# Kernel tuning notes

Hardware: AMD Instinct MI355X
Metric: run time of the kernel (lower is better)

The kernel has to match this reference:

```python
import jax, jax.numpy as jnp
import numpy as np

B, N, D = 256, 512, 128   # meta_batch, num_sample, feat_dim; in_c = 2*D = 256, base_c = 128
EPS_L1 = 1e-12
EPS_BN = 1e-5
NEG_SLOPE = 0.01


def setup_inputs() -> dict:
    key = jax.random.key(0)
    ks = jax.random.split(key, 6)
    return {
        "distribution_edge": jax.random.uniform(ks[0], (B, N, N), dtype=jnp.float32),
        "instance_edge": jax.random.uniform(ks[1], (B, N, N), dtype=jnp.float32),
        "point_node": jax.random.normal(ks[2], (B, N, D), dtype=jnp.float32),
        "W1": jax.random.normal(ks[3], (2 * D, 2 * D), dtype=jnp.float32) * 0.05,  # Conv2d 1x1: (out_c=base_c*2, in_c)
        "g1": jnp.ones((2 * D,), jnp.float32),
        "b1": jnp.zeros((2 * D,), jnp.float32),
        "W2": jax.random.normal(ks[4], (D, 2 * D), dtype=jnp.float32) * 0.05,     # Conv2d 1x1: (out_c=base_c, base_c*2)
        "g2": jnp.ones((D,), jnp.float32),
        "b2": jnp.zeros((D,), jnp.float32),
    }


def _l1_normalize(x):
    # F.normalize(x, p=1, dim=-1): x / max(sum(|x|, -1), 1e-12)
    return x / jnp.clip(jnp.sum(jnp.abs(x), axis=-1, keepdims=True), EPS_L1, None)


def _bn_lrelu(x, g, b):
    # x: (B, C, N); BatchNorm2d training-mode stats over (batch, spatial), biased var
    mean = jnp.mean(x, axis=(0, 2), keepdims=True)
    var = jnp.var(x, axis=(0, 2), keepdims=True)
    y = (x - mean) * jax.lax.rsqrt(var + EPS_BN) * g[None, :, None] + b[None, :, None]
    return jnp.where(y >= 0, y, NEG_SLOPE * y)


def reference(distribution_edge, instance_edge, point_node, W1, g1, b1, W2, g2, b2):
    n = point_node.shape[1]
    diag_mask = 1.0 - jnp.eye(n, dtype=point_node.dtype)  # broadcasts over meta_batch
    edge_feat = _l1_normalize(distribution_edge * diag_mask)
    aggr_feat = jnp.einsum('bij,bjd->bid', edge_feat, point_node)
    edge_instance = _l1_normalize(instance_edge * diag_mask)
    aggr_instance = jnp.einsum('bij,bjd->bid', edge_instance, point_node)
    x = jnp.concatenate([aggr_feat, aggr_instance], axis=-1)  # (B, N, 2D)
    x = jnp.swapaxes(x, 1, 2)                                  # (B, 2D, N)
    h = _bn_lrelu(jnp.einsum('oc,bcn->bon', W1, x), g1, b1)    # 1x1 conv, no bias
    h = _bn_lrelu(jnp.einsum('oc,bcn->bon', W2, h), g2, b2)
    return jnp.swapaxes(h, 1, 2)                               # (B, N, base_c)
```

## Files before the change

### kernel.cpp

```cpp
#include <hip/hip_runtime.h>
#include <hip/hip_bf16.h>
#include <string.h>

#define BB 256
#define NNS 512
#define DDF 128
#define CC1 256
#define CC2 128
#define NPOS (BB * NNS)

typedef __attribute__((ext_vector_type(4))) float f32x4;
typedef __attribute__((ext_vector_type(8))) short bf16x8;

__device__ __forceinline__ short f2bf(float f) {
    __hip_bfloat16 h = __float2bfloat16(f);
    short s;
    __builtin_memcpy(&s, &h, 2);
    return s;
}
__device__ __forceinline__ float bf2f(short s) {
    unsigned int u = ((unsigned int)(unsigned short)s) << 16;
    float f;
    __builtin_memcpy(&f, &u, 4);
    return f;
}
__device__ __forceinline__ unsigned int pk2bf(float a, float b) {
    float2 t; t.x = a; t.y = b;
    __hip_bfloat162 h = __float22bfloat162_rn(t);
    unsigned int u;
    __builtin_memcpy(&u, &h, 4);
    return u;
}

#define MFMA16(a, b, c) __builtin_amdgcn_mfma_f32_16x16x32_bf16(a, b, c, 0, 0, 0)

__global__ void prep_kernel(const float* __restrict__ W1, const float* __restrict__ W2,
                            short* __restrict__ W1b, short* __restrict__ W2b,
                            float* __restrict__ stats) {
    int idx = blockIdx.x * 256 + threadIdx.x;
    if (idx < CC1 * CC1) W1b[idx] = f2bf(W1[idx]);
    if (idx < CC2 * CC1) W2b[idx] = f2bf(W2[idx]);
    if (idx < 1536) stats[idx] = 0.0f;
}

__global__ __launch_bounds__(256) void transposeP_kernel(const float* __restrict__ P,
                                                         short* __restrict__ PT) {
    __shared__ float tp[64 * 132];
    int b = blockIdx.x >> 3;
    int j0 = (blockIdx.x & 7) * 64;
    int t = threadIdx.x;
    const float* Pb = P + ((size_t)b * NNS + j0) * DDF;
    int jr = t >> 5, dc = (t & 31) * 4;
#pragma unroll
    for (int p = 0; p < 8; ++p) {
        int j = p * 8 + jr;
        float4 v = *reinterpret_cast<const float4*>(&Pb[(size_t)j * DDF + dc]);
        *reinterpret_cast<float4*>(&tp[j * 132 + dc]) = v;
    }
    __syncthreads();
    int jo = t & 7;
#pragma unroll
    for (int p = 0; p < 4; ++p) {
        int d = p * 32 + (t >> 3);
        bf16x8 v;
#pragma unroll
        for (int s = 0; s < 8; ++s) v[s] = f2bf(tp[(jo * 8 + s) * 132 + d]);
        *reinterpret_cast<bf16x8*>(&PT[((size_t)(b * DDF + d)) * NNS + j0 + jo * 8]) = v;
    }
}

__global__ __launch_bounds__(256) void gemm1_kernel(const float* __restrict__ dE,
                                                    const float* __restrict__ iE,
                                                    const short* __restrict__ PT,
                                                    short* __restrict__ X) {
    int bid = blockIdx.x;
    int mtb = bid & 3;
    int e = (bid >> 2) & 1;
    int b = bid >> 3;
    const float* E = (e == 0 ? dE : iE) + (size_t)b * (NNS * NNS);
    const short* PTb = PT + (size_t)b * (DDF * NNS);

    int tid = threadIdx.x;
    int lane = tid & 63, w = tid >> 6;
    int quad = lane >> 4, lr = lane & 15;
    int rbase = mtb * 128 + w * 32;

    const float* Ap[2];
#pragma unroll
    for (int mt = 0; mt < 2; ++mt)
        Ap[mt] = E + (size_t)(rbase + mt * 16 + lr) * NNS + quad * 8;
    const short* Bp[8];
#pragma unroll
    for (int nt = 0; nt < 8; ++nt)
        Bp[nt] = PTb + (size_t)(nt * 16 + lr) * NNS + quad * 8;

    f32x4 zero = {0.f, 0.f, 0.f, 0.f};
    f32x4 acc[2][8];
#pragma unroll
    for (int a = 0; a < 2; ++a)
#pragma unroll
        for (int c = 0; c < 8; ++c) acc[a][c] = zero;
    float rs[2] = {0.f, 0.f};

    float4 pa0[2], pa1[2];
#pragma unroll
    for (int mt = 0; mt < 2; ++mt) {
        pa0[mt] = *reinterpret_cast<const float4*>(Ap[mt]);
        pa1[mt] = *reinterpret_cast<const float4*>(Ap[mt] + 4);
    }
    int kkd = rbase >> 5;

#pragma unroll 2
    for (int kk = 0; kk < 16; ++kk) {
        bf16x8 bv[8];
#pragma unroll
        for (int nt = 0; nt < 8; ++nt)
            bv[nt] = *reinterpret_cast<const bf16x8*>(Bp[nt] + kk * 32);
#pragma unroll
        for (int mt = 0; mt < 2; ++mt) {
            float4 v0 = pa0[mt], v1 = pa1[mt];
            if (kk < 15) {
                pa0[mt] = *reinterpret_cast<const float4*>(Ap[mt] + (kk + 1) * 32);
                pa1[mt] = *reinterpret_cast<const float4*>(Ap[mt] + (kk + 1) * 32 + 4);
            }
            float a8[8] = {v0.x, v0.y, v0.z, v0.w, v1.x, v1.y, v1.z, v1.w};
            if (kk == kkd) {
                int t = (mt << 4) + lr;
#pragma unroll
                for (int tt = 0; tt < 8; ++tt)
                    if (quad * 8 + tt == t) a8[tt] = 0.0f;
            }
            float s = rs[mt];
#pragma unroll
            for (int tt = 0; tt < 8; ++tt) s += fabsf(a8[tt]);
            rs[mt] = s;
            union { bf16x8 v; unsigned int u[4]; } af;
#pragma unroll
            for (int tt = 0; tt < 4; ++tt) af.u[tt] = pk2bf(a8[2 * tt], a8[2 * tt + 1]);
#pragma unroll
            for (int nt = 0; nt < 8; ++nt)
                acc[mt][nt] = MFMA16(af.v, bv[nt], acc[mt][nt]);
        }
    }

#pragma unroll
    for (int mt = 0; mt < 2; ++mt) {
        float s = rs[mt];
        s += __shfl_xor(s, 16, 64);
        s += __shfl_xor(s, 32, 64);
        float inv = 1.0f / fmaxf(s, 1e-12f);
        float ir[4];
#pragma unroll
        for (int r = 0; r < 4; ++r) ir[r] = __shfl(inv, quad * 4 + r, 64);
#pragma unroll
        for (int nt = 0; nt < 8; ++nt) {
            int col = e * 128 + nt * 16 + lr;
#pragma unroll
            for (int r = 0; r < 4; ++r) {
                int row = rbase + mt * 16 + quad * 4 + r;
                X[((size_t)b * NNS + row) * CC1 + col] = f2bf(acc[mt][nt][r] * ir[r]);
            }
        }
    }
}

__global__ __launch_bounds__(512) void gemm2_kernel(const short* __restrict__ X,
                                                    const short* __restrict__ W1b,
                                                    short* __restrict__ Y1,
                                                    float* __restrict__ sum1,
                                                    float* __restrict__ sumsq1) {
    int pbase = blockIdx.x * 128;
    int tid = threadIdx.x;
    int lane = tid & 63, w = tid >> 6;
    int quad = lane >> 4, lr = lane & 15;
    int mh = w >> 2, nh = w & 3;

    const short* Ap[4];
#pragma unroll
    for (int mt = 0; mt < 4; ++mt)
        Ap[mt] = X + (size_t)(pbase + mh * 64 + mt * 16 + lr) * CC1 + quad * 8;
    const short* Bp[4];
#pragma unroll
    for (int nt = 0; nt < 4; ++nt)
        Bp[nt] = W1b + (size_t)(nh * 64 + nt * 16 + lr) * CC1 + quad * 8;

    f32x4 zero = {0.f, 0.f, 0.f, 0.f};
    f32x4 acc[4][4];
#pragma unroll
    for (int a = 0; a < 4; ++a)
#pragma unroll
        for (int c = 0; c < 4; ++c) acc[a][c] = zero;

    bf16x8 pa[4];
#pragma unroll
    for (int mt = 0; mt < 4; ++mt) pa[mt] = *reinterpret_cast<const bf16x8*>(Ap[mt]);

#pragma unroll 2
    for (int kk = 0; kk < 8; ++kk) {
        bf16x8 bv[4];
#pragma unroll
        for (int nt = 0; nt < 4; ++nt)
            bv[nt] = *reinterpret_cast<const bf16x8*>(Bp[nt] + kk * 32);
#pragma unroll
        for (int mt = 0; mt < 4; ++mt) {
            bf16x8 av = pa[mt];
            if (kk < 7) pa[mt] = *reinterpret_cast<const bf16x8*>(Ap[mt] + (kk + 1) * 32);
#pragma unroll
            for (int nt = 0; nt < 4; ++nt) acc[mt][nt] = MFMA16(av, bv[nt], acc[mt][nt]);
        }
    }
#pragma unroll
    for (int nt = 0; nt < 4; ++nt) {
        int o = nh * 64 + nt * 16 + lr;
        float s = 0.f, q = 0.f;
#pragma unroll
        for (int mt = 0; mt < 4; ++mt)
#pragma unroll
            for (int r = 0; r < 4; ++r) {
                float v = acc[mt][nt][r];
                s += v;
                q += v * v;
            }
        s += __shfl_xor(s, 16, 64); s += __shfl_xor(s, 32, 64);
        q += __shfl_xor(q, 16, 64); q += __shfl_xor(q, 32, 64);
        if (lane < 16) {
            atomicAdd(&sum1[o], s);
            atomicAdd(&sumsq1[o], q);
        }
#pragma unroll
        for (int mt = 0; mt < 4; ++mt)
#pragma unroll
            for (int r = 0; r < 4; ++r) {
                int pos = pbase + mh * 64 + mt * 16 + quad * 4 + r;
                Y1[(size_t)pos * CC1 + o] = f2bf(acc[mt][nt][r]);
            }
    }
}

__global__ void finalize_kernel(const float* __restrict__ sum, const float* __restrict__ sumsq,
                                const float* __restrict__ g, const float* __restrict__ b,
                                float* __restrict__ scale, float* __restrict__ shift, int C) {
    int i = threadIdx.x;
    if (i < C) {
        const float invM = 1.0f / (float)NPOS;
        float m = sum[i] * invM;
        float v = sumsq[i] * invM - m * m;
        float s = g[i] * rsqrtf(v + 1e-5f);
        scale[i] = s;
        shift[i] = b[i] - m * s;
    }
}

__global__ __launch_bounds__(256) void gemm3_kernel(const short* __restrict__ Y1,
                                                    const short* __restrict__ W2b,
                                                    const float* __restrict__ scale1,
                                                    const float* __restrict__ shift1,
                                                    float* __restrict__ Y2,
                                                    float* __restrict__ sum2,
                                                    float* __restrict__ sumsq2) {
    __shared__ __align__(16) float ssc[CC1];
    __shared__ __align__(16) float ssh[CC1];
    ssc[threadIdx.x] = scale1[threadIdx.x];
    ssh[threadIdx.x] = shift1[threadIdx.x];
    __syncthreads();

    int pbase = blockIdx.x * 128;
    int tid = threadIdx.x;
    int lane = tid & 63, w = tid >> 6;
    int quad = lane >> 4, lr = lane & 15;
    int mh = w >> 1, nh = w & 1;

    const short* Ap[4];
#pragma unroll
    for (int mt = 0; mt < 4; ++mt)
        Ap[mt] = Y1 + (size_t)(pbase + mh * 64 + mt * 16 + lr) * CC1 + quad * 8;
    const short* Bp[4];
#pragma unroll
    for (int nt = 0; nt < 4; ++nt)
        Bp[nt] = W2b + (size_t)(nh * 64 + nt * 16 + lr) * CC1 + quad * 8;

    f32x4 zero = {0.f, 0.f, 0.f, 0.f};
    f32x4 acc[4][4];
#pragma unroll
    for (int a = 0; a < 4; ++a)
#pragma unroll
        for (int c = 0; c < 4; ++c) acc[a][c] = zero;

    bf16x8 pa[4];
#pragma unroll
    for (int mt = 0; mt < 4; ++mt) pa[mt] = *reinterpret_cast<const bf16x8*>(Ap[mt]);

#pragma unroll 2
    for (int kk = 0; kk < 8; ++kk) {
        bf16x8 bv[4];
#pragma unroll
        for (int nt = 0; nt < 4; ++nt)
            bv[nt] = *reinterpret_cast<const bf16x8*>(Bp[nt] + kk * 32);
        int k0 = kk * 32 + quad * 8;
        float4 sc0 = *reinterpret_cast<const float4*>(&ssc[k0]);
        float4 sc1 = *reinterpret_cast<const float4*>(&ssc[k0 + 4]);
        float4 sh0 = *reinterpret_cast<const float4*>(&ssh[k0]);
        float4 sh1 = *reinterpret_cast<const float4*>(&ssh[k0 + 4]);
        float scv[8] = {sc0.x, sc0.y, sc0.z, sc0.w, sc1.x, sc1.y, sc1.z, sc1.w};
        float shv[8] = {sh0.x, sh0.y, sh0.z, sh0.w, sh1.x, sh1.y, sh1.z, sh1.w};
#pragma unroll
        for (int mt = 0; mt < 4; ++mt) {
            bf16x8 raw = pa[mt];
            if (kk < 7) pa[mt] = *reinterpret_cast<const bf16x8*>(Ap[mt] + (kk + 1) * 32);
            union { bf16x8 v; unsigned int u[4]; } af;
#pragma unroll
            for (int tt = 0; tt < 4; ++tt) {
                float va = bf2f(raw[2 * tt]) * scv[2 * tt] + shv[2 * tt];
                va = fmaxf(va, 0.01f * va);
                float vb = bf2f(raw[2 * tt + 1]) * scv[2 * tt + 1] + shv[2 * tt + 1];
                vb = fmaxf(vb, 0.01f * vb);
                af.u[tt] = pk2bf(va, vb);
            }
#pragma unroll
            for (int nt = 0; nt < 4; ++nt) acc[mt][nt] = MFMA16(af.v, bv[nt], acc[mt][nt]);
        }
    }
#pragma unroll
    for (int nt = 0; nt < 4; ++nt) {
        int o = nh * 64 + nt * 16 + lr;
        float s = 0.f, q = 0.f;
#pragma unroll
        for (int mt = 0; mt < 4; ++mt)
#pragma unroll
            for (int r = 0; r < 4; ++r) {
                float v = acc[mt][nt][r];
                s += v;
                q += v * v;
            }
        s += __shfl_xor(s, 16, 64); s += __shfl_xor(s, 32, 64);
        q += __shfl_xor(q, 16, 64); q += __shfl_xor(q, 32, 64);
        if (lane < 16) {
            atomicAdd(&sum2[o], s);
            atomicAdd(&sumsq2[o], q);
        }
#pragma unroll
        for (int mt = 0; mt < 4; ++mt)
#pragma unroll
            for (int r = 0; r < 4; ++r) {
                int pos = pbase + mh * 64 + mt * 16 + quad * 4 + r;
                Y2[(size_t)pos * CC2 + o] = acc[mt][nt][r];
            }
    }
}

__global__ void apply2_kernel(const float* __restrict__ Y2, const float* __restrict__ scale2,
                              const float* __restrict__ shift2, float* __restrict__ out) {
    size_t gid = (size_t)blockIdx.x * 256 + threadIdx.x;
    size_t base = gid * 4;
    float4 y = *reinterpret_cast<const float4*>(&Y2[base]);
    int o = (int)(base & 127);
    float4 sc = *reinterpret_cast<const float4*>(&scale2[o]);
    float4 sh = *reinterpret_cast<const float4*>(&shift2[o]);
    float4 t;
    t.x = y.x * sc.x + sh.x; t.x = fmaxf(t.x, 0.01f * t.x);
    t.y = y.y * sc.y + sh.y; t.y = fmaxf(t.y, 0.01f * t.y);
    t.z = y.z * sc.z + sh.z; t.z = fmaxf(t.z, 0.01f * t.z);
    t.w = y.w * sc.w + sh.w; t.w = fmaxf(t.w, 0.01f * t.w);
    *reinterpret_cast<float4*>(&out[base]) = t;
}

extern "C" void kernel_launch(void* const* d_in, const int* in_sizes, int n_in,
                              void* d_out, int out_size, void* d_ws, size_t ws_size,
                              hipStream_t stream) {
    const float* dE = (const float*)d_in[0];
    const float* iE = (const float*)d_in[1];
    const float* P  = (const float*)d_in[2];
    const float* W1 = (const float*)d_in[3];
    const float* g1 = (const float*)d_in[4];
    const float* b1 = (const float*)d_in[5];
    const float* W2 = (const float*)d_in[6];
    const float* g2 = (const float*)d_in[7];
    const float* b2 = (const float*)d_in[8];
    float* out = (float*)d_out;
    char* ws = (char*)d_ws;

    short* PT  = (short*)(ws + 0);
    short* X   = (short*)(ws + 33554432);
    short* Y1  = (short*)(ws + 100663296);
    float* Y2  = (float*)(ws + 33554432);
    short* W1b = (short*)(ws + 167772160);
    short* W2b = (short*)(ws + 167903232);
    float* st  = (float*)(ws + 167968768);
    float* sum1 = st,        * sumsq1 = st + 256, * scale1 = st + 512,  * shift1 = st + 768;
    float* sum2 = st + 1024, * sumsq2 = st + 1152, * scale2 = st + 1280, * shift2 = st + 1408;

    prep_kernel<<<256, 256, 0, stream>>>(W1, W2, W1b, W2b, st);
    transposeP_kernel<<<2048, 256, 0, stream>>>(P, PT);
    gemm1_kernel<<<2048, 256, 0, stream>>>(dE, iE, PT, X);
    gemm2_kernel<<<1024, 512, 0, stream>>>(X, W1b, Y1, sum1, sumsq1);
    finalize_kernel<<<1, 256, 0, stream>>>(sum1, sumsq1, g1, b1, scale1, shift1, CC1);
    gemm3_kernel<<<1024, 256, 0, stream>>>(Y1, W2b, scale1, shift1, Y2, sum2, sumsq2);
    finalize_kernel<<<1, 128, 0, stream>>>(sum2, sumsq2, g2, b2, scale2, shift2, CC2);
    apply2_kernel<<<16384, 256, 0, stream>>>(Y2, scale2, shift2, out);
}
```

Measured before the change: 866.3 us.

## Shrink GEMM tiles and double-buffer operand loads in all three GEMM kernels

In the edge GEMM the four waves now split the tile into a 2x2 grid over rows and output columns, so each block covers 64 rows and 4096 blocks launch. The two pointwise GEMMs halve their row tile to 64 positions and launch twice as many blocks. All three kernels now prefetch A two k-steps ahead and B one step ahead into register double buffers, with the loops fully unrolled. The goal is to hide global-load latency and raise occupancy. The cost is that each edge row is now loaded by two waves, and the full unroll may increase register pressure.

```diff
diff --git a/kernel.cpp b/kernel.cpp
--- a/kernel.cpp
+++ b/kernel.cpp
@@ -74,55 +74,62 @@
                                                     const short* __restrict__ PT,
                                                     short* __restrict__ X) {
     int bid = blockIdx.x;
-    int mtb = bid & 3;
-    int e = (bid >> 2) & 1;
-    int b = bid >> 3;
+    int rt = bid & 7;
+    int e = (bid >> 3) & 1;
+    int b = bid >> 4;
     const float* E = (e == 0 ? dE : iE) + (size_t)b * (NNS * NNS);
     const short* PTb = PT + (size_t)b * (DDF * NNS);
 
     int tid = threadIdx.x;
     int lane = tid & 63, w = tid >> 6;
     int quad = lane >> 4, lr = lane & 15;
-    int rbase = mtb * 128 + w * 32;
+    int mh = w >> 1, nh = w & 1;
+    int rbase = rt * 64 + mh * 32;
 
     const float* Ap[2];
 #pragma unroll
     for (int mt = 0; mt < 2; ++mt)
         Ap[mt] = E + (size_t)(rbase + mt * 16 + lr) * NNS + quad * 8;
-    const short* Bp[8];
-#pragma unroll
-    for (int nt = 0; nt < 8; ++nt)
-        Bp[nt] = PTb + (size_t)(nt * 16 + lr) * NNS + quad * 8;
+    const short* Bp[4];
+#pragma unroll
+    for (int nt = 0; nt < 4; ++nt)
+        Bp[nt] = PTb + (size_t)(nh * 64 + nt * 16 + lr) * NNS + quad * 8;
 
     f32x4 zero = {0.f, 0.f, 0.f, 0.f};
-    f32x4 acc[2][8];
+    f32x4 acc[2][4];
 #pragma unroll
     for (int a = 0; a < 2; ++a)
 #pragma unroll
-        for (int c = 0; c < 8; ++c) acc[a][c] = zero;
+        for (int c = 0; c < 4; ++c) acc[a][c] = zero;
     float rs[2] = {0.f, 0.f};
 
-    float4 pa0[2], pa1[2];
+    float4 ab0[2][2], ab1[2][2];
+    bf16x8 bb[2][4];
 #pragma unroll
     for (int mt = 0; mt < 2; ++mt) {
-        pa0[mt] = *reinterpret_cast<const float4*>(Ap[mt]);
-        pa1[mt] = *reinterpret_cast<const float4*>(Ap[mt] + 4);
-    }
+        ab0[0][mt] = *reinterpret_cast<const float4*>(Ap[mt]);
+        ab1[0][mt] = *reinterpret_cast<const float4*>(Ap[mt] + 4);
+        ab0[1][mt] = *reinterpret_cast<const float4*>(Ap[mt] + 32);
+        ab1[1][mt] = *reinterpret_cast<const float4*>(Ap[mt] + 36);
+    }
+#pragma unroll
+    for (int nt = 0; nt < 4; ++nt)
+        bb[0][nt] = *reinterpret_cast<const bf16x8*>(Bp[nt]);
+
     int kkd = rbase >> 5;
 
-#pragma unroll 2
+#pragma unroll
     for (int kk = 0; kk < 16; ++kk) {
-        bf16x8 bv[8];
-#pragma unroll
-        for (int nt = 0; nt < 8; ++nt)
-            bv[nt] = *reinterpret_cast<const bf16x8*>(Bp[nt] + kk * 32);
+        int cb = kk & 1;
+        if (kk < 15) {
+#pragma unroll
+            for (int nt = 0; nt < 4; ++nt)
+                bb[cb ^ 1][nt] = *reinterpret_cast<const bf16x8*>(Bp[nt] + (kk + 1) * 32);
+        }
+        union { bf16x8 v; unsigned int u[4]; } af[2];
 #pragma unroll
         for (int mt = 0; mt < 2; ++mt) {
-            float4 v0 = pa0[mt], v1 = pa1[mt];
-            if (kk < 15) {
-                pa0[mt] = *reinterpret_cast<const float4*>(Ap[mt] + (kk + 1) * 32);
-                pa1[mt] = *reinterpret_cast<const float4*>(Ap[mt] + (kk + 1) * 32 + 4);
-            }
+            float4 v0 = ab0[cb][mt], v1 = ab1[cb][mt];
             float a8[8] = {v0.x, v0.y, v0.z, v0.w, v1.x, v1.y, v1.z, v1.w};
             if (kk == kkd) {
                 int t = (mt << 4) + lr;
@@ -134,13 +141,21 @@
 #pragma unroll
             for (int tt = 0; tt < 8; ++tt) s += fabsf(a8[tt]);
             rs[mt] = s;
-            union { bf16x8 v; unsigned int u[4]; } af;
-#pragma unroll
-            for (int tt = 0; tt < 4; ++tt) af.u[tt] = pk2bf(a8[2 * tt], a8[2 * tt + 1]);
-#pragma unroll
-            for (int nt = 0; nt < 8; ++nt)
-                acc[mt][nt] = MFMA16(af.v, bv[nt], acc[mt][nt]);
-        }
+#pragma unroll
+            for (int tt = 0; tt < 4; ++tt) af[mt].u[tt] = pk2bf(a8[2 * tt], a8[2 * tt + 1]);
+        }
+        if (kk < 14) {
+#pragma unroll
+            for (int mt = 0; mt < 2; ++mt) {
+                ab0[cb][mt] = *reinterpret_cast<const float4*>(Ap[mt] + (kk + 2) * 32);
+                ab1[cb][mt] = *reinterpret_cast<const float4*>(Ap[mt] + (kk + 2) * 32 + 4);
+            }
+        }
+#pragma unroll
+        for (int mt = 0; mt < 2; ++mt)
+#pragma unroll
+            for (int nt = 0; nt < 4; ++nt)
+                acc[mt][nt] = MFMA16(af[mt].v, bb[cb][nt], acc[mt][nt]);
     }
 
 #pragma unroll
@@ -153,8 +168,8 @@
 #pragma unroll
         for (int r = 0; r < 4; ++r) ir[r] = __shfl(inv, quad * 4 + r, 64);
 #pragma unroll
-        for (int nt = 0; nt < 8; ++nt) {
-            int col = e * 128 + nt * 16 + lr;
+        for (int nt = 0; nt < 4; ++nt) {
+            int col = e * 128 + nh * 64 + nt * 16 + lr;
 #pragma unroll
             for (int r = 0; r < 4; ++r) {
                 int row = rbase + mt * 16 + quad * 4 + r;
@@ -169,52 +184,66 @@
                                                     short* __restrict__ Y1,
                                                     float* __restrict__ sum1,
                                                     float* __restrict__ sumsq1) {
-    int pbase = blockIdx.x * 128;
+    int pbase = blockIdx.x * 64;
     int tid = threadIdx.x;
     int lane = tid & 63, w = tid >> 6;
     int quad = lane >> 4, lr = lane & 15;
     int mh = w >> 2, nh = w & 3;
 
-    const short* Ap[4];
-#pragma unroll
-    for (int mt = 0; mt < 4; ++mt)
-        Ap[mt] = X + (size_t)(pbase + mh * 64 + mt * 16 + lr) * CC1 + quad * 8;
+    const short* Ap[2];
+#pragma unroll
+    for (int mt = 0; mt < 2; ++mt)
+        Ap[mt] = X + (size_t)(pbase + mh * 32 + mt * 16 + lr) * CC1 + quad * 8;
     const short* Bp[4];
 #pragma unroll
     for (int nt = 0; nt < 4; ++nt)
         Bp[nt] = W1b + (size_t)(nh * 64 + nt * 16 + lr) * CC1 + quad * 8;
 
     f32x4 zero = {0.f, 0.f, 0.f, 0.f};
-    f32x4 acc[4][4];
-#pragma unroll
-    for (int a = 0; a < 4; ++a)
+    f32x4 acc[2][4];
+#pragma unroll
+    for (int a = 0; a < 2; ++a)
 #pragma unroll
         for (int c = 0; c < 4; ++c) acc[a][c] = zero;
 
-    bf16x8 pa[4];
-#pragma unroll
-    for (int mt = 0; mt < 4; ++mt) pa[mt] = *reinterpret_cast<const bf16x8*>(Ap[mt]);
-
-#pragma unroll 2
+    bf16x8 ab[2][2], bb[2][4];
+#pragma unroll
+    for (int mt = 0; mt < 2; ++mt) {
+        ab[0][mt] = *reinterpret_cast<const bf16x8*>(Ap[mt]);
+        ab[1][mt] = *reinterpret_cast<const bf16x8*>(Ap[mt] + 32);
+    }
+#pragma unroll
+    for (int nt = 0; nt < 4; ++nt)
+        bb[0][nt] = *reinterpret_cast<const bf16x8*>(Bp[nt]);
+
+#pragma unroll
     for (int kk = 0; kk < 8; ++kk) {
-        bf16x8 bv[4];
-#pragma unroll
-        for (int nt = 0; nt < 4; ++nt)
-            bv[nt] = *reinterpret_cast<const bf16x8*>(Bp[nt] + kk * 32);
-#pragma unroll
-        for (int mt = 0; mt < 4; ++mt) {
-            bf16x8 av = pa[mt];
-            if (kk < 7) pa[mt] = *reinterpret_cast<const bf16x8*>(Ap[mt] + (kk + 1) * 32);
-#pragma unroll
-            for (int nt = 0; nt < 4; ++nt) acc[mt][nt] = MFMA16(av, bv[nt], acc[mt][nt]);
-        }
+        int cb = kk & 1;
+        if (kk < 7) {
+#pragma unroll
+            for (int nt = 0; nt < 4; ++nt)
+                bb[cb ^ 1][nt] = *reinterpret_cast<const bf16x8*>(Bp[nt] + (kk + 1) * 32);
+        }
+        bf16x8 av[2];
+#pragma unroll
+        for (int mt = 0; mt < 2; ++mt) av[mt] = ab[cb][mt];
+        if (kk < 6) {
+#pragma unroll
+            for (int mt = 0; mt < 2; ++mt)
+                ab[cb][mt] = *reinterpret_cast<const bf16x8*>(Ap[mt] + (kk + 2) * 32);
+        }
+#pragma unroll
+        for (int mt = 0; mt < 2; ++mt)
+#pragma unroll
+            for (int nt = 0; nt < 4; ++nt)
+                acc[mt][nt] = MFMA16(av[mt], bb[cb][nt], acc[mt][nt]);
     }
 #pragma unroll
     for (int nt = 0; nt < 4; ++nt) {
         int o = nh * 64 + nt * 16 + lr;
         float s = 0.f, q = 0.f;
 #pragma unroll
-        for (int mt = 0; mt < 4; ++mt)
+        for (int mt = 0; mt < 2; ++mt)
 #pragma unroll
             for (int r = 0; r < 4; ++r) {
                 float v = acc[mt][nt][r];
@@ -228,10 +257,10 @@
             atomicAdd(&sumsq1[o], q);
         }
 #pragma unroll
-        for (int mt = 0; mt < 4; ++mt)
+        for (int mt = 0; mt < 2; ++mt)
 #pragma unroll
             for (int r = 0; r < 4; ++r) {
-                int pos = pbase + mh * 64 + mt * 16 + quad * 4 + r;
+                int pos = pbase + mh * 32 + mt * 16 + quad * 4 + r;
                 Y1[(size_t)pos * CC1 + o] = f2bf(acc[mt][nt][r]);
             }
     }
@@ -264,38 +293,46 @@
     ssh[threadIdx.x] = shift1[threadIdx.x];
     __syncthreads();
 
-    int pbase = blockIdx.x * 128;
+    int pbase = blockIdx.x * 64;
     int tid = threadIdx.x;
     int lane = tid & 63, w = tid >> 6;
     int quad = lane >> 4, lr = lane & 15;
     int mh = w >> 1, nh = w & 1;
 
-    const short* Ap[4];
-#pragma unroll
-    for (int mt = 0; mt < 4; ++mt)
-        Ap[mt] = Y1 + (size_t)(pbase + mh * 64 + mt * 16 + lr) * CC1 + quad * 8;
+    const short* Ap[2];
+#pragma unroll
+    for (int mt = 0; mt < 2; ++mt)
+        Ap[mt] = Y1 + (size_t)(pbase + mh * 32 + mt * 16 + lr) * CC1 + quad * 8;
     const short* Bp[4];
 #pragma unroll
     for (int nt = 0; nt < 4; ++nt)
         Bp[nt] = W2b + (size_t)(nh * 64 + nt * 16 + lr) * CC1 + quad * 8;
 
     f32x4 zero = {0.f, 0.f, 0.f, 0.f};
-    f32x4 acc[4][4];
-#pragma unroll
-    for (int a = 0; a < 4; ++a)
+    f32x4 acc[2][4];
+#pragma unroll
+    for (int a = 0; a < 2; ++a)
 #pragma unroll
         for (int c = 0; c < 4; ++c) acc[a][c] = zero;
 
-    bf16x8 pa[4];
-#pragma unroll
-    for (int mt = 0; mt < 4; ++mt) pa[mt] = *reinterpret_cast<const bf16x8*>(Ap[mt]);
-
-#pragma unroll 2
+    bf16x8 ab[2][2], bb[2][4];
+#pragma unroll
+    for (int mt = 0; mt < 2; ++mt) {
+        ab[0][mt] = *reinterpret_cast<const bf16x8*>(Ap[mt]);
+        ab[1][mt] = *reinterpret_cast<const bf16x8*>(Ap[mt] + 32);
+    }
+#pragma unroll
+    for (int nt = 0; nt < 4; ++nt)
+        bb[0][nt] = *reinterpret_cast<const bf16x8*>(Bp[nt]);
+
+#pragma unroll
     for (int kk = 0; kk < 8; ++kk) {
-        bf16x8 bv[4];
-#pragma unroll
-        for (int nt = 0; nt < 4; ++nt)
-            bv[nt] = *reinterpret_cast<const bf16x8*>(Bp[nt] + kk * 32);
+        int cb = kk & 1;
+        if (kk < 7) {
+#pragma unroll
+            for (int nt = 0; nt < 4; ++nt)
+                bb[cb ^ 1][nt] = *reinterpret_cast<const bf16x8*>(Bp[nt] + (kk + 1) * 32);
+        }
         int k0 = kk * 32 + quad * 8;
         float4 sc0 = *reinterpret_cast<const float4*>(&ssc[k0]);
         float4 sc1 = *reinterpret_cast<const float4*>(&ssc[k0 + 4]);
@@ -303,29 +340,36 @@
         float4 sh1 = *reinterpret_cast<const float4*>(&ssh[k0 + 4]);
         float scv[8] = {sc0.x, sc0.y, sc0.z, sc0.w, sc1.x, sc1.y, sc1.z, sc1.w};
         float shv[8] = {sh0.x, sh0.y, sh0.z, sh0.w, sh1.x, sh1.y, sh1.z, sh1.w};
-#pragma unroll
-        for (int mt = 0; mt < 4; ++mt) {
-            bf16x8 raw = pa[mt];
-            if (kk < 7) pa[mt] = *reinterpret_cast<const bf16x8*>(Ap[mt] + (kk + 1) * 32);
-            union { bf16x8 v; unsigned int u[4]; } af;
+        union { bf16x8 v; unsigned int u[4]; } af[2];
+#pragma unroll
+        for (int mt = 0; mt < 2; ++mt) {
+            bf16x8 raw = ab[cb][mt];
 #pragma unroll
             for (int tt = 0; tt < 4; ++tt) {
                 float va = bf2f(raw[2 * tt]) * scv[2 * tt] + shv[2 * tt];
                 va = fmaxf(va, 0.01f * va);
                 float vb = bf2f(raw[2 * tt + 1]) * scv[2 * tt + 1] + shv[2 * tt + 1];
                 vb = fmaxf(vb, 0.01f * vb);
-                af.u[tt] = pk2bf(va, vb);
-            }
-#pragma unroll
-            for (int nt = 0; nt < 4; ++nt) acc[mt][nt] = MFMA16(af.v, bv[nt], acc[mt][nt]);
-        }
+                af[mt].u[tt] = pk2bf(va, vb);
+            }
+        }
+        if (kk < 6) {
+#pragma unroll
+            for (int mt = 0; mt < 2; ++mt)
+                ab[cb][mt] = *reinterpret_cast<const bf16x8*>(Ap[mt] + (kk + 2) * 32);
+        }
+#pragma unroll
+        for (int mt = 0; mt < 2; ++mt)
+#pragma unroll
+            for (int nt = 0; nt < 4; ++nt)
+                acc[mt][nt] = MFMA16(af[mt].v, bb[cb][nt], acc[mt][nt]);
     }
 #pragma unroll
     for (int nt = 0; nt < 4; ++nt) {
         int o = nh * 64 + nt * 16 + lr;
         float s = 0.f, q = 0.f;
 #pragma unroll
-        for (int mt = 0; mt < 4; ++mt)
+        for (int mt = 0; mt < 2; ++mt)
 #pragma unroll
             for (int r = 0; r < 4; ++r) {
                 float v = acc[mt][nt][r];
@@ -339,10 +383,10 @@
             atomicAdd(&sumsq2[o], q);
         }
 #pragma unroll
-        for (int mt = 0; mt < 4; ++mt)
+        for (int mt = 0; mt < 2; ++mt)
 #pragma unroll
             for (int r = 0; r < 4; ++r) {
-                int pos = pbase + mh * 64 + mt * 16 + quad * 4 + r;
+                int pos = pbase + mh * 32 + mt * 16 + quad * 4 + r;
                 Y2[(size_t)pos * CC2 + o] = acc[mt][nt][r];
             }
     }
@@ -391,10 +435,10 @@
 
     prep_kernel<<<256, 256, 0, stream>>>(W1, W2, W1b, W2b, st);
     transposeP_kernel<<<2048, 256, 0, stream>>>(P, PT);
-    gemm1_kernel<<<2048, 256, 0, stream>>>(dE, iE, PT, X);
-    gemm2_kernel<<<1024, 512, 0, stream>>>(X, W1b, Y1, sum1, sumsq1);
+    gemm1_kernel<<<4096, 256, 0, stream>>>(dE, iE, PT, X);
+    gemm2_kernel<<<2048, 512, 0, stream>>>(X, W1b, Y1, sum1, sumsq1);
     finalize_kernel<<<1, 256, 0, stream>>>(sum1, sumsq1, g1, b1, scale1, shift1, CC1);
-    gemm3_kernel<<<1024, 256, 0, stream>>>(Y1, W2b, scale1, shift1, Y2, sum2, sumsq2);
+    gemm3_kernel<<<2048, 256, 0, stream>>>(Y1, W2b, scale1, shift1, Y2, sum2, sumsq2);
     finalize_kernel<<<1, 128, 0, stream>>>(sum2, sumsq2, g2, b2, scale2, shift2, CC2);
     apply2_kernel<<<16384, 256, 0, stream>>>(Y2, scale2, shift2, out);
 }
```

New measurement: 984.1 us. 13.6% more time.
